# Kernel tuning notes

Measured on AMD Instinct MI355X. Metric: run time of the kernel, lower is better.

Reference implementation:

```python
import jax, jax.numpy as jnp
import numpy as np
import math

D_MODEL = 512
NUM_HEADS = 8
D_K = D_MODEL // NUM_HEADS
MAX_LEN = 500
BATCH = 32
SEQ = 480


def setup_inputs() -> dict:
    key = jax.random.key(0)
    ks = jax.random.split(key, 10)
    s = 0.02
    x = jax.random.normal(ks[0], (BATCH, SEQ, D_MODEL), dtype=jnp.float32)
    wq = jax.random.normal(ks[1], (D_MODEL, D_MODEL), dtype=jnp.float32) * s
    bq = jnp.zeros((D_MODEL,), jnp.float32)
    wk = jax.random.normal(ks[2], (D_MODEL, D_MODEL), dtype=jnp.float32) * s
    bk = jnp.zeros((D_MODEL,), jnp.float32)
    wv = jax.random.normal(ks[3], (D_MODEL, D_MODEL), dtype=jnp.float32) * s
    bv = jnp.zeros((D_MODEL,), jnp.float32)
    wo = jax.random.normal(ks[4], (D_MODEL, D_MODEL), dtype=jnp.float32) * s
    bo = jnp.zeros((D_MODEL,), jnp.float32)
    rel_bias = jax.random.normal(ks[5], (NUM_HEADS, MAX_LEN, MAX_LEN), dtype=jnp.float32) * 0.02
    return {"x": x, "wq": wq, "bq": bq, "wk": wk, "bk": bk, "wv": wv,
            "bv": bv, "wo": wo, "bo": bo, "rel_bias": rel_bias}


def reference(x, wq, bq, wk, bk, wv, bv, wo, bo, rel_bias):
    B, S, D = x.shape
    H, dk = NUM_HEADS, D_K
    scale = math.sqrt(dk)
    # QKV projections -> [B, H, S, dk]
    q = (x @ wq + bq).reshape(B, S, H, dk).transpose(0, 2, 1, 3)
    k = (x @ wk + bk).reshape(B, S, H, dk).transpose(0, 2, 1, 3)
    v = (x @ wv + bv).reshape(B, S, H, dk).transpose(0, 2, 1, 3)
    scores = jnp.einsum('bhqd,bhkd->bhqk', q, k) / scale
    scores = scores + rel_bias[None, :, :S, :S]
    causal = jnp.triu(jnp.ones((S, S), dtype=bool), k=1)  # True where j > i
    scores = jnp.where(causal[None, None], -jnp.inf, scores)
    attn = jax.nn.softmax(scores, axis=-1)
    ctx = jnp.einsum('bhqk,bhkd->bhqd', attn, v)
    ctx = ctx.transpose(0, 2, 1, 3).reshape(B, S, D)
    out = ctx @ wo + bo
    return out, attn.mean(axis=1)
```

## Files before the change

### kernel.cpp

```cpp
#include <hip/hip_runtime.h>
#include <hip/hip_bf16.h>


typedef unsigned short ushort_t;
typedef __attribute__((ext_vector_type(8))) short short8;
typedef __attribute__((ext_vector_type(4))) float floatx4;
typedef __attribute__((ext_vector_type(2))) __fp16 half2v;

#define NB 32
#define NS 480
#define ND 512
#define NH 8
#define NDK 64
#define MAXLEN 500
#define PSTR 36
#define SCL 0.18033688f

__device__ __forceinline__ ushort_t f2bf(float f) {
  union { float f; unsigned u; } v; v.f = f;
  unsigned r = v.u + 0x7FFFu + ((v.u >> 16) & 1u);
  return (ushort_t)(r >> 16);
}

#define GLOAD_LDS16(g, l)                                                      \
  __builtin_amdgcn_global_load_lds(                                            \
      (const __attribute__((address_space(1))) void*)(g),                      \
      (__attribute__((address_space(3))) void*)(l), 16, 0, 0)

__global__ void cvt_x(const float* __restrict__ x, ushort_t* __restrict__ xb) {
  int idx = blockIdx.x * 256 + threadIdx.x;
  float4 v = ((const float4*)x)[idx];
  ushort4 o;
  o.x = f2bf(v.x); o.y = f2bf(v.y); o.z = f2bf(v.z); o.w = f2bf(v.w);
  ((ushort4*)xb)[idx] = o;
}

__global__ void cvt_w(const float* __restrict__ wq, const float* __restrict__ wk,
                      const float* __restrict__ wv, const float* __restrict__ wo,
                      ushort_t* __restrict__ wqT, ushort_t* __restrict__ wkT,
                      ushort_t* __restrict__ wvT, ushort_t* __restrict__ woT) {
  __shared__ float t[32][33];
  int z = blockIdx.z;
  const float* w = (z == 0) ? wq : (z == 1) ? wk : (z == 2) ? wv : wo;
  ushort_t* wT = (z == 0) ? wqT : (z == 1) ? wkT : (z == 2) ? wvT : woT;
  int k0 = blockIdx.x * 32, n0 = blockIdx.y * 32;
  int tx = threadIdx.x & 31, ty = threadIdx.x >> 5;
#pragma unroll
  for (int yy = 0; yy < 4; ++yy)
    t[ty + yy * 8][tx] = w[(k0 + ty + yy * 8) * ND + n0 + tx];
  __syncthreads();
#pragma unroll
  for (int yy = 0; yy < 4; ++yy)
    wT[(n0 + ty + yy * 8) * ND + k0 + tx] = f2bf(t[tx][ty + yy * 8]);
}

__global__ void cvt_rbt(const float* __restrict__ rel_bias, float* __restrict__ rbt) {
  int kt = blockIdx.x, ib = blockIdx.y, h = blockIdx.z;
  int lm = threadIdx.x & 15, ii = threadIdx.x >> 4;
  int i = ib * 16 + ii;
  float f0 = rel_bias[((size_t)h * MAXLEN + i) * MAXLEN + kt * 32 + lm] * 1.44269504f;
  float f1 = rel_bias[((size_t)h * MAXLEN + i) * MAXLEN + kt * 32 + 16 + lm] * 1.44269504f;
  float2 o = {f0, f1};
  *(float2*)&rbt[(((size_t)h * 15 + kt) * NS + i) * 32 + 2 * lm] = o;
}

__global__ __launch_bounds__(256)
void qk_gemm(const ushort_t* __restrict__ xb,
             const ushort_t* __restrict__ wqT, const ushort_t* __restrict__ wkT,
             const float* __restrict__ bq, const float* __restrict__ bk,
             ushort_t* __restrict__ qb, ushort_t* __restrict__ kb) {
  __shared__ __align__(16) ushort_t sA[128 * 64];
  __shared__ __align__(16) ushort_t sB[128 * 64];
  const int tid = threadIdx.x;
  const int wid = tid >> 6, lane = tid & 63;
  const int lm = lane & 15, quad = lane >> 4;
  const int wr = wid >> 1, wc = wid & 1;
  const int row0 = blockIdx.x * 128;
  const int col0 = blockIdx.y * 128;
  const int z = blockIdx.z;
  const ushort_t* Bt = (z == 0) ? wqT : wkT;
  const float* bias = (z == 0) ? bq : bk;

  floatx4 zero4 = {0.f, 0.f, 0.f, 0.f};
  floatx4 acc[4][4];
#pragma unroll
  for (int i = 0; i < 4; ++i)
#pragma unroll
    for (int j = 0; j < 4; ++j) acc[i][j] = zero4;

  for (int k0 = 0; k0 < ND; k0 += 64) {
#pragma unroll
    for (int c = 0; c < 4; ++c) {
      int li = c * 256 + tid;
      int row = li >> 3, kc = li & 7;
      int kcs = kc ^ (row & 7);
      GLOAD_LDS16(xb + (row0 + row) * ND + k0 + kcs * 8, sA + (c * 256 + wid * 64) * 8);
      GLOAD_LDS16(Bt + (col0 + row) * ND + k0 + kcs * 8, sB + (c * 256 + wid * 64) * 8);
    }
    __syncthreads();
#pragma unroll
    for (int h2 = 0; h2 < 2; ++h2) {
      short8 a[4], b[4];
#pragma unroll
      for (int i = 0; i < 4; ++i) {
        int row = wr * 64 + i * 16 + lm;
        a[i] = *(const short8*)&sA[row * 64 + (((h2 << 2) | quad) ^ (lm & 7)) * 8];
      }
#pragma unroll
      for (int j = 0; j < 4; ++j) {
        int row = wc * 64 + j * 16 + lm;
        b[j] = *(const short8*)&sB[row * 64 + (((h2 << 2) | quad) ^ (lm & 7)) * 8];
      }
#pragma unroll
      for (int i = 0; i < 4; ++i)
#pragma unroll
        for (int j = 0; j < 4; ++j)
          acc[i][j] = __builtin_amdgcn_mfma_f32_16x16x32_bf16(a[i], b[j], acc[i][j], 0, 0, 0);
    }
    __syncthreads();
  }

  float bsv[4];
#pragma unroll
  for (int j = 0; j < 4; ++j) bsv[j] = bias[col0 + wc * 64 + j * 16 + lm];

#pragma unroll
  for (int i = 0; i < 4; ++i)
#pragma unroll
    for (int j = 0; j < 4; ++j)
#pragma unroll
      for (int r = 0; r < 4; ++r) {
        int m = row0 + wr * 64 + i * 16 + quad * 4 + r;
        int n = col0 + wc * 64 + j * 16 + lm;
        float val = acc[i][j][r] + bsv[j];
        int bb = m / NS, s = m - bb * NS;
        int h = n >> 6, d = n & 63;
        ushort_t o = f2bf(val);
        if (z == 0) qb[((bb * NH + h) * NS + s) * NDK + d] = o;
        else        kb[((bb * NH + h) * NS + s) * NDK + d] = o;
      }
}

__global__ __launch_bounds__(256)
void v_gemm(const ushort_t* __restrict__ xb, const ushort_t* __restrict__ wvT,
            const float* __restrict__ bv, ushort_t* __restrict__ vtil) {
  __shared__ __align__(16) ushort_t sA[128 * 64];
  __shared__ __align__(16) ushort_t sB[128 * 64];
  const int tid = threadIdx.x;
  const int wid = tid >> 6, lane = tid & 63;
  const int lm = lane & 15, quad = lane >> 4;
  const int wr = wid >> 1, wc = wid & 1;
  const int row0 = blockIdx.x * 128;
  const int col0 = blockIdx.y * 128;
  const int b = blockIdx.z;
  const ushort_t* xbb = xb + (size_t)b * NS * ND;

  floatx4 zero4 = {0.f, 0.f, 0.f, 0.f};
  floatx4 acc[4][4];
#pragma unroll
  for (int i = 0; i < 4; ++i)
#pragma unroll
    for (int j = 0; j < 4; ++j) acc[i][j] = zero4;

  for (int k0 = 0; k0 < ND; k0 += 64) {
#pragma unroll
    for (int c = 0; c < 4; ++c) {
      int li = c * 256 + tid;
      int row = li >> 3, kc = li & 7;
      int kcs = kc ^ (row & 7);
      GLOAD_LDS16(wvT + (row0 + row) * ND + k0 + kcs * 8, sA + (c * 256 + wid * 64) * 8);
      int srow = min(col0 + row, NS - 1);
      GLOAD_LDS16(xbb + srow * ND + k0 + kcs * 8, sB + (c * 256 + wid * 64) * 8);
    }
    __syncthreads();
#pragma unroll
    for (int h2 = 0; h2 < 2; ++h2) {
      short8 a[4], b2[4];
#pragma unroll
      for (int i = 0; i < 4; ++i) {
        int row = wr * 64 + i * 16 + lm;
        a[i] = *(const short8*)&sA[row * 64 + (((h2 << 2) | quad) ^ (lm & 7)) * 8];
      }
#pragma unroll
      for (int j = 0; j < 4; ++j) {
        int row = wc * 64 + j * 16 + lm;
        b2[j] = *(const short8*)&sB[row * 64 + (((h2 << 2) | quad) ^ (lm & 7)) * 8];
      }
#pragma unroll
      for (int i = 0; i < 4; ++i)
#pragma unroll
        for (int j = 0; j < 4; ++j)
          acc[i][j] = __builtin_amdgcn_mfma_f32_16x16x32_bf16(a[i], b2[j], acc[i][j], 0, 0, 0);
    }
    __syncthreads();
  }

#pragma unroll
  for (int i = 0; i < 4; ++i)
#pragma unroll
    for (int r = 0; r < 4; ++r) {
      int m = row0 + wr * 64 + i * 16 + quad * 4 + r;
      float bias = bv[m];
#pragma unroll
      for (int j = 0; j < 4; ++j) {
        int n = col0 + wc * 64 + j * 16 + lm;
        if (n < NS) {
          size_t idx = (((size_t)b * NH + (m >> 6)) * 15 + (n >> 5)) * 2048 +
                       (m & 63) * 32 + (n & 31);
          vtil[idx] = f2bf(acc[i][j][r] + bias);
        }
      }
    }
}

__global__ __launch_bounds__(256)
void flash_attn(const ushort_t* __restrict__ qb, const ushort_t* __restrict__ kb,
                const ushort_t* __restrict__ vtil, const float* __restrict__ rbt,
                ushort_t* __restrict__ ctxb, float* __restrict__ cst,
                uint4* __restrict__ pscr) {
  const int bh = blockIdx.x;
  const int b = bh >> 3, h = bh & 7;
  const int tid = threadIdx.x;
  const int wid = tid >> 6, lane = tid & 63;
  const int lm = lane & 15, quad = lane >> 4;

  __shared__ __align__(16) ushort_t sP[4][32 * PSTR];

  const int t = 14 - (blockIdx.y * 4 + wid);
  if (t < 0) return;
  const int nkt = t + 1;

  const ushort_t* qh = qb + (size_t)bh * NS * NDK;
  const ushort_t* kh = kb + (size_t)bh * NS * NDK;
  const ushort_t* vb = vtil + (size_t)bh * 15 * 2048;
  const float* rb = rbt + (size_t)h * 15 * NS * 32;
  uint4* pp = pscr + ((size_t)(bh * 120 + (t * (t + 1)) / 2)) * 128 + lane;

  short8 aq[2][2];
#pragma unroll
  for (int g = 0; g < 2; ++g) {
    aq[g][0] = *(const short8*)&qh[(t * 32 + g * 16 + lm) * NDK + quad * 8];
    aq[g][1] = *(const short8*)&qh[(t * 32 + g * 16 + lm) * NDK + 32 + quad * 8];
  }

  float lsum[2][4];
  floatx4 O[2][4];
  floatx4 zero4 = {0.f, 0.f, 0.f, 0.f};
#pragma unroll
  for (int g = 0; g < 2; ++g) {
#pragma unroll
    for (int r = 0; r < 4; ++r) lsum[g][r] = 0.f;
#pragma unroll
    for (int jd = 0; jd < 4; ++jd) O[g][jd] = zero4;
  }

  for (int kt = 0; kt < nkt; ++kt) {
    const int kvA = kt * 32 + lm;
    const int kvB = kvA + 16;
    short8 bkA0 = *(const short8*)&kh[kvA * NDK + quad * 8];
    short8 bkA1 = *(const short8*)&kh[kvA * NDK + 32 + quad * 8];
    short8 bkB0 = *(const short8*)&kh[kvB * NDK + quad * 8];
    short8 bkB1 = *(const short8*)&kh[kvB * NDK + 32 + quad * 8];
    short8 bv2[4];
#pragma unroll
    for (int jd = 0; jd < 4; ++jd)
      bv2[jd] = *(const short8*)&vb[kt * 2048 + (jd * 16 + lm) * 32 + quad * 8];
    float2 bb[2][4];
#pragma unroll
    for (int g = 0; g < 2; ++g)
#pragma unroll
      for (int r = 0; r < 4; ++r) {
        int i = t * 32 + g * 16 + quad * 4 + r;
        bb[g][r] = *(const float2*)&rb[((size_t)kt * NS + i) * 32 + 2 * lm];
      }

    floatx4 sA[2], sB[2];
    __builtin_amdgcn_s_setprio(1);
#pragma unroll
    for (int g = 0; g < 2; ++g) {
      floatx4 s = zero4;
      s = __builtin_amdgcn_mfma_f32_16x16x32_bf16(aq[g][0], bkA0, s, 0, 0, 0);
      s = __builtin_amdgcn_mfma_f32_16x16x32_bf16(aq[g][1], bkA1, s, 0, 0, 0);
      sA[g] = s;
      s = zero4;
      s = __builtin_amdgcn_mfma_f32_16x16x32_bf16(aq[g][0], bkB0, s, 0, 0, 0);
      s = __builtin_amdgcn_mfma_f32_16x16x32_bf16(aq[g][1], bkB1, s, 0, 0, 0);
      sB[g] = s;
    }
    __builtin_amdgcn_s_setprio(0);

    const bool diag = (kt == t);
#pragma unroll
    for (int g = 0; g < 2; ++g) {
      unsigned pw[4];
#pragma unroll
      for (int r = 0; r < 4; ++r) {
        float p0 = __builtin_amdgcn_exp2f(fmaf(sA[g][r], SCL, bb[g][r].x));
        float p1 = __builtin_amdgcn_exp2f(fmaf(sB[g][r], SCL, bb[g][r].y));
        if (diag) {
          int i = t * 32 + g * 16 + quad * 4 + r;
          if (kvA > i) p0 = 0.f;
          if (kvB > i) p1 = 0.f;
        }
        lsum[g][r] += p0 + p1;
        unsigned pk;
        asm("v_cvt_pk_bf16_f32 %0, %1, %2" : "=v"(pk) : "v"(p0), "v"(p1));
        sP[wid][(g * 16 + quad * 4 + r) * PSTR + lm] = (ushort_t)(pk & 0xffffu);
        sP[wid][(g * 16 + quad * 4 + r) * PSTR + 16 + lm] = (ushort_t)(pk >> 16);
        half2v hp = __builtin_amdgcn_cvt_pkrtz(p0, p1);
        pw[r] = *(unsigned*)&hp;
      }
      uint4 pq = {pw[0], pw[1], pw[2], pw[3]};
      pp[(size_t)kt * 128 + g * 64] = pq;
    }

    __builtin_amdgcn_s_setprio(1);
#pragma unroll
    for (int g = 0; g < 2; ++g) {
      short8 ap = *(const short8*)&sP[wid][(g * 16 + lm) * PSTR + quad * 8];
#pragma unroll
      for (int jd = 0; jd < 4; ++jd)
        O[g][jd] = __builtin_amdgcn_mfma_f32_16x16x32_bf16(ap, bv2[jd], O[g][jd], 0, 0, 0);
    }
    __builtin_amdgcn_s_setprio(0);
  }

#pragma unroll
  for (int off = 1; off < 16; off <<= 1)
#pragma unroll
    for (int g = 0; g < 2; ++g)
#pragma unroll
      for (int r = 0; r < 4; ++r) lsum[g][r] += __shfl_xor(lsum[g][r], off, 64);

#pragma unroll
  for (int g = 0; g < 2; ++g) {
    float rinv[4];
#pragma unroll
    for (int r = 0; r < 4; ++r) rinv[r] = 1.f / lsum[g][r];
#pragma unroll
    for (int jd = 0; jd < 4; ++jd)
#pragma unroll
      for (int r = 0; r < 4; ++r) {
        int i = t * 32 + g * 16 + quad * 4 + r;
        ctxb[((size_t)b * NS + i) * ND + h * NDK + jd * 16 + lm] =
            f2bf(O[g][jd][r] * rinv[r]);
      }
    if (lm == 0) {
#pragma unroll
      for (int r = 0; r < 4; ++r) {
        int i = t * 32 + g * 16 + quad * 4 + r;
        cst[(size_t)bh * NS + i] = rinv[r];
      }
    }
  }
}

__global__ __launch_bounds__(64)
void attn_mean_p(const uint4* __restrict__ pscr, const float* __restrict__ cst,
                 float* __restrict__ am) {
  const int b = blockIdx.x, t = blockIdx.y, kt = blockIdx.z;
  const int lane = threadIdx.x;
  const int lm = lane & 15, quad = lane >> 4;
  float* outp = am + ((size_t)b * NS + t * 32) * NS + (size_t)kt * 32;
  if (kt > t) {
#pragma unroll
    for (int g = 0; g < 2; ++g)
#pragma unroll
      for (int r = 0; r < 4; ++r) {
        int row = g * 16 + quad * 4 + r;
        outp[(size_t)row * NS + lm] = 0.f;
        outp[(size_t)row * NS + 16 + lm] = 0.f;
      }
    return;
  }
  const int m = (t * (t + 1)) / 2 + kt;
  float a0[2][4], a1[2][4];
#pragma unroll
  for (int g = 0; g < 2; ++g)
#pragma unroll
    for (int r = 0; r < 4; ++r) { a0[g][r] = 0.f; a1[g][r] = 0.f; }

#pragma unroll
  for (int h = 0; h < NH; ++h) {
    const uint4* pp = pscr + ((size_t)(b * NH + h) * 120 + m) * 128 + lane;
    uint4 q0 = pp[0];
    uint4 q1 = pp[64];
    unsigned pu[8] = {q0.x, q0.y, q0.z, q0.w, q1.x, q1.y, q1.z, q1.w};
    const float* cp = cst + (size_t)(b * NH + h) * NS + t * 32 + quad * 4;
    float4 rv0 = *(const float4*)cp;
    float4 rv1 = *(const float4*)(cp + 16);
    float rv[8] = {rv0.x, rv0.y, rv0.z, rv0.w, rv1.x, rv1.y, rv1.z, rv1.w};
#pragma unroll
    for (int g = 0; g < 2; ++g)
#pragma unroll
      for (int r = 0; r < 4; ++r) {
        half2v hp = *(half2v*)&pu[g * 4 + r];
        a0[g][r] = fmaf((float)hp.x, rv[g * 4 + r], a0[g][r]);
        a1[g][r] = fmaf((float)hp.y, rv[g * 4 + r], a1[g][r]);
      }
  }

#pragma unroll
  for (int g = 0; g < 2; ++g)
#pragma unroll
    for (int r = 0; r < 4; ++r) {
      int row = g * 16 + quad * 4 + r;
      outp[(size_t)row * NS + lm] = a0[g][r] * 0.125f;
      outp[(size_t)row * NS + 16 + lm] = a1[g][r] * 0.125f;
    }
}

__global__ __launch_bounds__(256)
void out_gemm(const ushort_t* __restrict__ ctxb, const ushort_t* __restrict__ woT,
              const float* __restrict__ bo, float* __restrict__ out) {
  __shared__ __align__(16) ushort_t sA[128 * 64];
  __shared__ __align__(16) ushort_t sB[128 * 64];
  const int tid = threadIdx.x;
  const int wid = tid >> 6, lane = tid & 63;
  const int lm = lane & 15, quad = lane >> 4;
  const int wr = wid >> 1, wc = wid & 1;
  const int row0 = blockIdx.x * 128;
  const int col0 = blockIdx.y * 128;

  floatx4 zero4 = {0.f, 0.f, 0.f, 0.f};
  floatx4 acc[4][4];
#pragma unroll
  for (int i = 0; i < 4; ++i)
#pragma unroll
    for (int j = 0; j < 4; ++j) acc[i][j] = zero4;

  for (int k0 = 0; k0 < ND; k0 += 64) {
#pragma unroll
    for (int c = 0; c < 4; ++c) {
      int li = c * 256 + tid;
      int row = li >> 3, kc = li & 7;
      int kcs = kc ^ (row & 7);
      GLOAD_LDS16(ctxb + (row0 + row) * ND + k0 + kcs * 8, sA + (c * 256 + wid * 64) * 8);
      GLOAD_LDS16(woT + (col0 + row) * ND + k0 + kcs * 8, sB + (c * 256 + wid * 64) * 8);
    }
    __syncthreads();
#pragma unroll
    for (int h2 = 0; h2 < 2; ++h2) {
      short8 a[4], b[4];
#pragma unroll
      for (int i = 0; i < 4; ++i) {
        int row = wr * 64 + i * 16 + lm;
        a[i] = *(const short8*)&sA[row * 64 + (((h2 << 2) | quad) ^ (lm & 7)) * 8];
      }
#pragma unroll
      for (int j = 0; j < 4; ++j) {
        int row = wc * 64 + j * 16 + lm;
        b[j] = *(const short8*)&sB[row * 64 + (((h2 << 2) | quad) ^ (lm & 7)) * 8];
      }
#pragma unroll
      for (int i = 0; i < 4; ++i)
#pragma unroll
        for (int j = 0; j < 4; ++j)
          acc[i][j] = __builtin_amdgcn_mfma_f32_16x16x32_bf16(a[i], b[j], acc[i][j], 0, 0, 0);
    }
    __syncthreads();
  }

  float bsv[4];
#pragma unroll
  for (int j = 0; j < 4; ++j) bsv[j] = bo[col0 + wc * 64 + j * 16 + lm];

#pragma unroll
  for (int i = 0; i < 4; ++i)
#pragma unroll
    for (int j = 0; j < 4; ++j)
#pragma unroll
      for (int r = 0; r < 4; ++r) {
        int m = row0 + wr * 64 + i * 16 + quad * 4 + r;
        int n = col0 + wc * 64 + j * 16 + lm;
        out[m * ND + n] = acc[i][j][r] + bsv[j];
      }
}

extern "C" void kernel_launch(void* const* d_in, const int* in_sizes, int n_in,
                              void* d_out, int out_size, void* d_ws, size_t ws_size,
                              hipStream_t stream) {
  const float* x  = (const float*)d_in[0];
  const float* wq = (const float*)d_in[1];
  const float* bq = (const float*)d_in[2];
  const float* wk = (const float*)d_in[3];
  const float* bk = (const float*)d_in[4];
  const float* wv = (const float*)d_in[5];
  const float* bv = (const float*)d_in[6];
  const float* wo = (const float*)d_in[7];
  const float* bo = (const float*)d_in[8];
  const float* rel_bias = (const float*)d_in[9];

  char* w = (char*)d_ws;
  ushort_t* xb  = (ushort_t*)w;
  ushort_t* wqT = (ushort_t*)(w + 15728640);
  ushort_t* wkT = wqT + 262144;
  ushort_t* wvT = wkT + 262144;
  ushort_t* woT = wvT + 262144;
  ushort_t* qb  = (ushort_t*)(w + 15728640 + 4 * 524288);
  ushort_t* kb  = qb + 7864320;
  ushort_t* vtil = kb + 7864320;
  ushort_t* ctxb = vtil + 7864320;
  float* cstat = (float*)(w + 80740352);
  uint4* pscr = (uint4*)(w + 81264640);
  float* rbt = (float*)w;

  float* out0 = (float*)d_out;
  float* attn_mean = out0 + 7864320;

  cvt_x<<<dim3(7680), dim3(256), 0, stream>>>(x, xb);
  cvt_w<<<dim3(16, 16, 4), dim3(256), 0, stream>>>(wq, wk, wv, wo, wqT, wkT, wvT, woT);
  qk_gemm<<<dim3(120, 4, 2), dim3(256), 0, stream>>>(xb, wqT, wkT, bq, bk, qb, kb);
  v_gemm<<<dim3(4, 4, 32), dim3(256), 0, stream>>>(xb, wvT, bv, vtil);
  cvt_rbt<<<dim3(15, 30, 8), dim3(256), 0, stream>>>(rel_bias, rbt);
  flash_attn<<<dim3(256, 4), dim3(256), 0, stream>>>(qb, kb, vtil, rbt, ctxb, cstat, pscr);
  attn_mean_p<<<dim3(32, 15, 15), dim3(64), 0, stream>>>(pscr, cstat, attn_mean);
  out_gemm<<<dim3(120, 4), dim3(256), 0, stream>>>(ctxb, woT, bo, out0);
}
```

Baseline: 230.9 us.

## Fuse conversion and QKV GEMM launches; pair causal query tiles per wave

Merges the x and weight bf16 conversion kernels into one launch, and the Q/K and V projection GEMMs into one launch dispatched on blockIdx.z. In flash attention each wave now processes two query tiles (t and 13-t, with one slot taking the last tile), so every wave does an equal amount of causal work and the grid is halved. The aim is to cut launch overhead and causal load imbalance, at the cost of fewer concurrent waves for latency hiding and some idle padding blocks in the fused GEMM.

```diff
diff --git a/kernel.cpp b/kernel.cpp
--- a/kernel.cpp
+++ b/kernel.cpp
@@ -27,23 +27,27 @@
       (const __attribute__((address_space(1))) void*)(g),                      \
       (__attribute__((address_space(3))) void*)(l), 16, 0, 0)
 
-__global__ void cvt_x(const float* __restrict__ x, ushort_t* __restrict__ xb) {
-  int idx = blockIdx.x * 256 + threadIdx.x;
-  float4 v = ((const float4*)x)[idx];
-  ushort4 o;
-  o.x = f2bf(v.x); o.y = f2bf(v.y); o.z = f2bf(v.z); o.w = f2bf(v.w);
-  ((ushort4*)xb)[idx] = o;
-}
-
-__global__ void cvt_w(const float* __restrict__ wq, const float* __restrict__ wk,
-                      const float* __restrict__ wv, const float* __restrict__ wo,
-                      ushort_t* __restrict__ wqT, ushort_t* __restrict__ wkT,
-                      ushort_t* __restrict__ wvT, ushort_t* __restrict__ woT) {
+__global__ __launch_bounds__(256)
+void cvt_xw(const float* __restrict__ x, const float* __restrict__ wq,
+            const float* __restrict__ wk, const float* __restrict__ wv,
+            const float* __restrict__ wo, ushort_t* __restrict__ xb,
+            ushort_t* __restrict__ wqT, ushort_t* __restrict__ wkT,
+            ushort_t* __restrict__ wvT, ushort_t* __restrict__ woT) {
   __shared__ float t[32][33];
-  int z = blockIdx.z;
+  const int bid = blockIdx.x;
+  if (bid < 7680) {
+    int idx = bid * 256 + threadIdx.x;
+    float4 v = ((const float4*)x)[idx];
+    ushort4 o;
+    o.x = f2bf(v.x); o.y = f2bf(v.y); o.z = f2bf(v.z); o.w = f2bf(v.w);
+    ((ushort4*)xb)[idx] = o;
+    return;
+  }
+  const int q = bid - 7680;
+  const int z = q >> 8;
   const float* w = (z == 0) ? wq : (z == 1) ? wk : (z == 2) ? wv : wo;
   ushort_t* wT = (z == 0) ? wqT : (z == 1) ? wkT : (z == 2) ? wvT : woT;
-  int k0 = blockIdx.x * 32, n0 = blockIdx.y * 32;
+  int k0 = (q & 15) * 32, n0 = ((q >> 4) & 15) * 32;
   int tx = threadIdx.x & 31, ty = threadIdx.x >> 5;
 #pragma unroll
   for (int yy = 0; yy < 4; ++yy)
@@ -65,21 +69,20 @@
 }
 
 __global__ __launch_bounds__(256)
-void qk_gemm(const ushort_t* __restrict__ xb,
-             const ushort_t* __restrict__ wqT, const ushort_t* __restrict__ wkT,
-             const float* __restrict__ bq, const float* __restrict__ bk,
-             ushort_t* __restrict__ qb, ushort_t* __restrict__ kb) {
+void qkv_gemm(const ushort_t* __restrict__ xb,
+              const ushort_t* __restrict__ wqT, const ushort_t* __restrict__ wkT,
+              const ushort_t* __restrict__ wvT,
+              const float* __restrict__ bq, const float* __restrict__ bk,
+              const float* __restrict__ bv,
+              ushort_t* __restrict__ qb, ushort_t* __restrict__ kb,
+              ushort_t* __restrict__ vtil) {
   __shared__ __align__(16) ushort_t sA[128 * 64];
   __shared__ __align__(16) ushort_t sB[128 * 64];
   const int tid = threadIdx.x;
   const int wid = tid >> 6, lane = tid & 63;
   const int lm = lane & 15, quad = lane >> 4;
   const int wr = wid >> 1, wc = wid & 1;
-  const int row0 = blockIdx.x * 128;
-  const int col0 = blockIdx.y * 128;
   const int z = blockIdx.z;
-  const ushort_t* Bt = (z == 0) ? wqT : wkT;
-  const float* bias = (z == 0) ? bq : bk;
 
   floatx4 zero4 = {0.f, 0.f, 0.f, 0.f};
   floatx4 acc[4][4];
@@ -88,129 +91,120 @@
 #pragma unroll
     for (int j = 0; j < 4; ++j) acc[i][j] = zero4;
 
-  for (int k0 = 0; k0 < ND; k0 += 64) {
-#pragma unroll
-    for (int c = 0; c < 4; ++c) {
-      int li = c * 256 + tid;
-      int row = li >> 3, kc = li & 7;
-      int kcs = kc ^ (row & 7);
-      GLOAD_LDS16(xb + (row0 + row) * ND + k0 + kcs * 8, sA + (c * 256 + wid * 64) * 8);
-      GLOAD_LDS16(Bt + (col0 + row) * ND + k0 + kcs * 8, sB + (c * 256 + wid * 64) * 8);
-    }
-    __syncthreads();
-#pragma unroll
-    for (int h2 = 0; h2 < 2; ++h2) {
-      short8 a[4], b[4];
-#pragma unroll
-      for (int i = 0; i < 4; ++i) {
-        int row = wr * 64 + i * 16 + lm;
-        a[i] = *(const short8*)&sA[row * 64 + (((h2 << 2) | quad) ^ (lm & 7)) * 8];
-      }
-#pragma unroll
-      for (int j = 0; j < 4; ++j) {
-        int row = wc * 64 + j * 16 + lm;
-        b[j] = *(const short8*)&sB[row * 64 + (((h2 << 2) | quad) ^ (lm & 7)) * 8];
-      }
-#pragma unroll
-      for (int i = 0; i < 4; ++i)
-#pragma unroll
-        for (int j = 0; j < 4; ++j)
-          acc[i][j] = __builtin_amdgcn_mfma_f32_16x16x32_bf16(a[i], b[j], acc[i][j], 0, 0, 0);
-    }
-    __syncthreads();
-  }
-
-  float bsv[4];
-#pragma unroll
-  for (int j = 0; j < 4; ++j) bsv[j] = bias[col0 + wc * 64 + j * 16 + lm];
-
-#pragma unroll
-  for (int i = 0; i < 4; ++i)
-#pragma unroll
-    for (int j = 0; j < 4; ++j)
+  if (z < 2) {
+    if (blockIdx.x >= 120) return;
+    const int row0 = blockIdx.x * 128;
+    const int col0 = blockIdx.y * 128;
+    const ushort_t* Bt = (z == 0) ? wqT : wkT;
+    const float* bias = (z == 0) ? bq : bk;
+
+    for (int k0 = 0; k0 < ND; k0 += 64) {
+#pragma unroll
+      for (int c = 0; c < 4; ++c) {
+        int li = c * 256 + tid;
+        int row = li >> 3, kc = li & 7;
+        int kcs = kc ^ (row & 7);
+        GLOAD_LDS16(xb + (row0 + row) * ND + k0 + kcs * 8, sA + (c * 256 + wid * 64) * 8);
+        GLOAD_LDS16(Bt + (col0 + row) * ND + k0 + kcs * 8, sB + (c * 256 + wid * 64) * 8);
+      }
+      __syncthreads();
+#pragma unroll
+      for (int h2 = 0; h2 < 2; ++h2) {
+        short8 a[4], b[4];
+#pragma unroll
+        for (int i = 0; i < 4; ++i) {
+          int row = wr * 64 + i * 16 + lm;
+          a[i] = *(const short8*)&sA[row * 64 + (((h2 << 2) | quad) ^ (lm & 7)) * 8];
+        }
+#pragma unroll
+        for (int j = 0; j < 4; ++j) {
+          int row = wc * 64 + j * 16 + lm;
+          b[j] = *(const short8*)&sB[row * 64 + (((h2 << 2) | quad) ^ (lm & 7)) * 8];
+        }
+#pragma unroll
+        for (int i = 0; i < 4; ++i)
+#pragma unroll
+          for (int j = 0; j < 4; ++j)
+            acc[i][j] = __builtin_amdgcn_mfma_f32_16x16x32_bf16(a[i], b[j], acc[i][j], 0, 0, 0);
+      }
+      __syncthreads();
+    }
+
+    float bsv[4];
+#pragma unroll
+    for (int j = 0; j < 4; ++j) bsv[j] = bias[col0 + wc * 64 + j * 16 + lm];
+
+#pragma unroll
+    for (int i = 0; i < 4; ++i)
+#pragma unroll
+      for (int j = 0; j < 4; ++j)
+#pragma unroll
+        for (int r = 0; r < 4; ++r) {
+          int m = row0 + wr * 64 + i * 16 + quad * 4 + r;
+          int n = col0 + wc * 64 + j * 16 + lm;
+          float val = acc[i][j][r] + bsv[j];
+          int bb = m / NS, s = m - bb * NS;
+          int h = n >> 6, d = n & 63;
+          ushort_t o = f2bf(val);
+          if (z == 0) qb[((bb * NH + h) * NS + s) * NDK + d] = o;
+          else        kb[((bb * NH + h) * NS + s) * NDK + d] = o;
+        }
+  } else {
+    const int b = blockIdx.x >> 2;
+    const int row0 = (blockIdx.x & 3) * 128;
+    const int col0 = blockIdx.y * 128;
+    const ushort_t* xbb = xb + (size_t)b * NS * ND;
+
+    for (int k0 = 0; k0 < ND; k0 += 64) {
+#pragma unroll
+      for (int c = 0; c < 4; ++c) {
+        int li = c * 256 + tid;
+        int row = li >> 3, kc = li & 7;
+        int kcs = kc ^ (row & 7);
+        GLOAD_LDS16(wvT + (row0 + row) * ND + k0 + kcs * 8, sA + (c * 256 + wid * 64) * 8);
+        int srow = min(col0 + row, NS - 1);
+        GLOAD_LDS16(xbb + srow * ND + k0 + kcs * 8, sB + (c * 256 + wid * 64) * 8);
+      }
+      __syncthreads();
+#pragma unroll
+      for (int h2 = 0; h2 < 2; ++h2) {
+        short8 a[4], b2[4];
+#pragma unroll
+        for (int i = 0; i < 4; ++i) {
+          int row = wr * 64 + i * 16 + lm;
+          a[i] = *(const short8*)&sA[row * 64 + (((h2 << 2) | quad) ^ (lm & 7)) * 8];
+        }
+#pragma unroll
+        for (int j = 0; j < 4; ++j) {
+          int row = wc * 64 + j * 16 + lm;
+          b2[j] = *(const short8*)&sB[row * 64 + (((h2 << 2) | quad) ^ (lm & 7)) * 8];
+        }
+#pragma unroll
+        for (int i = 0; i < 4; ++i)
+#pragma unroll
+          for (int j = 0; j < 4; ++j)
+            acc[i][j] = __builtin_amdgcn_mfma_f32_16x16x32_bf16(a[i], b2[j], acc[i][j], 0, 0, 0);
+      }
+      __syncthreads();
+    }
+
+#pragma unroll
+    for (int i = 0; i < 4; ++i)
 #pragma unroll
       for (int r = 0; r < 4; ++r) {
         int m = row0 + wr * 64 + i * 16 + quad * 4 + r;
-        int n = col0 + wc * 64 + j * 16 + lm;
-        float val = acc[i][j][r] + bsv[j];
-        int bb = m / NS, s = m - bb * NS;
-        int h = n >> 6, d = n & 63;
-        ushort_t o = f2bf(val);
-        if (z == 0) qb[((bb * NH + h) * NS + s) * NDK + d] = o;
-        else        kb[((bb * NH + h) * NS + s) * NDK + d] = o;
-      }
-}
-
-__global__ __launch_bounds__(256)
-void v_gemm(const ushort_t* __restrict__ xb, const ushort_t* __restrict__ wvT,
-            const float* __restrict__ bv, ushort_t* __restrict__ vtil) {
-  __shared__ __align__(16) ushort_t sA[128 * 64];
-  __shared__ __align__(16) ushort_t sB[128 * 64];
-  const int tid = threadIdx.x;
-  const int wid = tid >> 6, lane = tid & 63;
-  const int lm = lane & 15, quad = lane >> 4;
-  const int wr = wid >> 1, wc = wid & 1;
-  const int row0 = blockIdx.x * 128;
-  const int col0 = blockIdx.y * 128;
-  const int b = blockIdx.z;
-  const ushort_t* xbb = xb + (size_t)b * NS * ND;
-
-  floatx4 zero4 = {0.f, 0.f, 0.f, 0.f};
-  floatx4 acc[4][4];
-#pragma unroll
-  for (int i = 0; i < 4; ++i)
-#pragma unroll
-    for (int j = 0; j < 4; ++j) acc[i][j] = zero4;
-
-  for (int k0 = 0; k0 < ND; k0 += 64) {
-#pragma unroll
-    for (int c = 0; c < 4; ++c) {
-      int li = c * 256 + tid;
-      int row = li >> 3, kc = li & 7;
-      int kcs = kc ^ (row & 7);
-      GLOAD_LDS16(wvT + (row0 + row) * ND + k0 + kcs * 8, sA + (c * 256 + wid * 64) * 8);
-      int srow = min(col0 + row, NS - 1);
-      GLOAD_LDS16(xbb + srow * ND + k0 + kcs * 8, sB + (c * 256 + wid * 64) * 8);
-    }
-    __syncthreads();
-#pragma unroll
-    for (int h2 = 0; h2 < 2; ++h2) {
-      short8 a[4], b2[4];
-#pragma unroll
-      for (int i = 0; i < 4; ++i) {
-        int row = wr * 64 + i * 16 + lm;
-        a[i] = *(const short8*)&sA[row * 64 + (((h2 << 2) | quad) ^ (lm & 7)) * 8];
-      }
-#pragma unroll
-      for (int j = 0; j < 4; ++j) {
-        int row = wc * 64 + j * 16 + lm;
-        b2[j] = *(const short8*)&sB[row * 64 + (((h2 << 2) | quad) ^ (lm & 7)) * 8];
-      }
-#pragma unroll
-      for (int i = 0; i < 4; ++i)
-#pragma unroll
-        for (int j = 0; j < 4; ++j)
-          acc[i][j] = __builtin_amdgcn_mfma_f32_16x16x32_bf16(a[i], b2[j], acc[i][j], 0, 0, 0);
-    }
-    __syncthreads();
+        float bias = bv[m];
+#pragma unroll
+        for (int j = 0; j < 4; ++j) {
+          int n = col0 + wc * 64 + j * 16 + lm;
+          if (n < NS) {
+            size_t idx = (((size_t)b * NH + (m >> 6)) * 15 + (n >> 5)) * 2048 +
+                         (m & 63) * 32 + (n & 31);
+            vtil[idx] = f2bf(acc[i][j][r] + bias);
+          }
+        }
+      }
   }
-
-#pragma unroll
-  for (int i = 0; i < 4; ++i)
-#pragma unroll
-    for (int r = 0; r < 4; ++r) {
-      int m = row0 + wr * 64 + i * 16 + quad * 4 + r;
-      float bias = bv[m];
-#pragma unroll
-      for (int j = 0; j < 4; ++j) {
-        int n = col0 + wc * 64 + j * 16 + lm;
-        if (n < NS) {
-          size_t idx = (((size_t)b * NH + (m >> 6)) * 15 + (n >> 5)) * 2048 +
-                       (m & 63) * 32 + (n & 31);
-          vtil[idx] = f2bf(acc[i][j][r] + bias);
-        }
-      }
-    }
 }
 
 __global__ __launch_bounds__(256)
@@ -226,130 +220,137 @@
 
   __shared__ __align__(16) ushort_t sP[4][32 * PSTR];
 
-  const int t = 14 - (blockIdx.y * 4 + wid);
-  if (t < 0) return;
-  const int nkt = t + 1;
+  const int slot = blockIdx.y * 4 + wid;
+  const int tA = (slot == 7) ? 14 : slot;
+  const int tB = (slot == 7) ? -1 : 13 - slot;
 
   const ushort_t* qh = qb + (size_t)bh * NS * NDK;
   const ushort_t* kh = kb + (size_t)bh * NS * NDK;
   const ushort_t* vb = vtil + (size_t)bh * 15 * 2048;
   const float* rb = rbt + (size_t)h * 15 * NS * 32;
-  uint4* pp = pscr + ((size_t)(bh * 120 + (t * (t + 1)) / 2)) * 128 + lane;
-
-  short8 aq[2][2];
-#pragma unroll
-  for (int g = 0; g < 2; ++g) {
-    aq[g][0] = *(const short8*)&qh[(t * 32 + g * 16 + lm) * NDK + quad * 8];
-    aq[g][1] = *(const short8*)&qh[(t * 32 + g * 16 + lm) * NDK + 32 + quad * 8];
-  }
-
-  float lsum[2][4];
-  floatx4 O[2][4];
-  floatx4 zero4 = {0.f, 0.f, 0.f, 0.f};
-#pragma unroll
-  for (int g = 0; g < 2; ++g) {
-#pragma unroll
-    for (int r = 0; r < 4; ++r) lsum[g][r] = 0.f;
-#pragma unroll
-    for (int jd = 0; jd < 4; ++jd) O[g][jd] = zero4;
-  }
-
-  for (int kt = 0; kt < nkt; ++kt) {
-    const int kvA = kt * 32 + lm;
-    const int kvB = kvA + 16;
-    short8 bkA0 = *(const short8*)&kh[kvA * NDK + quad * 8];
-    short8 bkA1 = *(const short8*)&kh[kvA * NDK + 32 + quad * 8];
-    short8 bkB0 = *(const short8*)&kh[kvB * NDK + quad * 8];
-    short8 bkB1 = *(const short8*)&kh[kvB * NDK + 32 + quad * 8];
-    short8 bv2[4];
-#pragma unroll
-    for (int jd = 0; jd < 4; ++jd)
-      bv2[jd] = *(const short8*)&vb[kt * 2048 + (jd * 16 + lm) * 32 + quad * 8];
-    float2 bb[2][4];
-#pragma unroll
-    for (int g = 0; g < 2; ++g)
-#pragma unroll
-      for (int r = 0; r < 4; ++r) {
-        int i = t * 32 + g * 16 + quad * 4 + r;
-        bb[g][r] = *(const float2*)&rb[((size_t)kt * NS + i) * 32 + 2 * lm];
-      }
-
-    floatx4 sA[2], sB[2];
-    __builtin_amdgcn_s_setprio(1);
+
+#pragma unroll 1
+  for (int ti = 0; ti < 2; ++ti) {
+    const int t = (ti == 0) ? tA : tB;
+    if (t < 0) break;
+    const int nkt = t + 1;
+    uint4* pp = pscr + ((size_t)(bh * 120 + (t * (t + 1)) / 2)) * 128 + lane;
+
+    short8 aq[2][2];
 #pragma unroll
     for (int g = 0; g < 2; ++g) {
-      floatx4 s = zero4;
-      s = __builtin_amdgcn_mfma_f32_16x16x32_bf16(aq[g][0], bkA0, s, 0, 0, 0);
-      s = __builtin_amdgcn_mfma_f32_16x16x32_bf16(aq[g][1], bkA1, s, 0, 0, 0);
-      sA[g] = s;
-      s = zero4;
-      s = __builtin_amdgcn_mfma_f32_16x16x32_bf16(aq[g][0], bkB0, s, 0, 0, 0);
-      s = __builtin_amdgcn_mfma_f32_16x16x32_bf16(aq[g][1], bkB1, s, 0, 0, 0);
-      sB[g] = s;
-    }
-    __builtin_amdgcn_s_setprio(0);
-
-    const bool diag = (kt == t);
+      aq[g][0] = *(const short8*)&qh[(t * 32 + g * 16 + lm) * NDK + quad * 8];
+      aq[g][1] = *(const short8*)&qh[(t * 32 + g * 16 + lm) * NDK + 32 + quad * 8];
+    }
+
+    float lsum[2][4];
+    floatx4 O[2][4];
+    floatx4 zero4 = {0.f, 0.f, 0.f, 0.f};
 #pragma unroll
     for (int g = 0; g < 2; ++g) {
-      unsigned pw[4];
-#pragma unroll
-      for (int r = 0; r < 4; ++r) {
-        float p0 = __builtin_amdgcn_exp2f(fmaf(sA[g][r], SCL, bb[g][r].x));
-        float p1 = __builtin_amdgcn_exp2f(fmaf(sB[g][r], SCL, bb[g][r].y));
-        if (diag) {
+#pragma unroll
+      for (int r = 0; r < 4; ++r) lsum[g][r] = 0.f;
+#pragma unroll
+      for (int jd = 0; jd < 4; ++jd) O[g][jd] = zero4;
+    }
+
+    for (int kt = 0; kt < nkt; ++kt) {
+      const int kvA = kt * 32 + lm;
+      const int kvB = kvA + 16;
+      short8 bkA0 = *(const short8*)&kh[kvA * NDK + quad * 8];
+      short8 bkA1 = *(const short8*)&kh[kvA * NDK + 32 + quad * 8];
+      short8 bkB0 = *(const short8*)&kh[kvB * NDK + quad * 8];
+      short8 bkB1 = *(const short8*)&kh[kvB * NDK + 32 + quad * 8];
+      short8 bv2[4];
+#pragma unroll
+      for (int jd = 0; jd < 4; ++jd)
+        bv2[jd] = *(const short8*)&vb[kt * 2048 + (jd * 16 + lm) * 32 + quad * 8];
+      float2 bb[2][4];
+#pragma unroll
+      for (int g = 0; g < 2; ++g)
+#pragma unroll
+        for (int r = 0; r < 4; ++r) {
           int i = t * 32 + g * 16 + quad * 4 + r;
-          if (kvA > i) p0 = 0.f;
-          if (kvB > i) p1 = 0.f;
-        }
-        lsum[g][r] += p0 + p1;
-        unsigned pk;
-        asm("v_cvt_pk_bf16_f32 %0, %1, %2" : "=v"(pk) : "v"(p0), "v"(p1));
-        sP[wid][(g * 16 + quad * 4 + r) * PSTR + lm] = (ushort_t)(pk & 0xffffu);
-        sP[wid][(g * 16 + quad * 4 + r) * PSTR + 16 + lm] = (ushort_t)(pk >> 16);
-        half2v hp = __builtin_amdgcn_cvt_pkrtz(p0, p1);
-        pw[r] = *(unsigned*)&hp;
-      }
-      uint4 pq = {pw[0], pw[1], pw[2], pw[3]};
-      pp[(size_t)kt * 128 + g * 64] = pq;
-    }
-
-    __builtin_amdgcn_s_setprio(1);
+          bb[g][r] = *(const float2*)&rb[((size_t)kt * NS + i) * 32 + 2 * lm];
+        }
+
+      floatx4 sA[2], sB[2];
+      __builtin_amdgcn_s_setprio(1);
+#pragma unroll
+      for (int g = 0; g < 2; ++g) {
+        floatx4 s = zero4;
+        s = __builtin_amdgcn_mfma_f32_16x16x32_bf16(aq[g][0], bkA0, s, 0, 0, 0);
+        s = __builtin_amdgcn_mfma_f32_16x16x32_bf16(aq[g][1], bkA1, s, 0, 0, 0);
+        sA[g] = s;
+        s = zero4;
+        s = __builtin_amdgcn_mfma_f32_16x16x32_bf16(aq[g][0], bkB0, s, 0, 0, 0);
+        s = __builtin_amdgcn_mfma_f32_16x16x32_bf16(aq[g][1], bkB1, s, 0, 0, 0);
+        sB[g] = s;
+      }
+      __builtin_amdgcn_s_setprio(0);
+
+      const bool diag = (kt == t);
+#pragma unroll
+      for (int g = 0; g < 2; ++g) {
+        unsigned pw[4];
+#pragma unroll
+        for (int r = 0; r < 4; ++r) {
+          float p0 = __builtin_amdgcn_exp2f(fmaf(sA[g][r], SCL, bb[g][r].x));
+          float p1 = __builtin_amdgcn_exp2f(fmaf(sB[g][r], SCL, bb[g][r].y));
+          if (diag) {
+            int i = t * 32 + g * 16 + quad * 4 + r;
+            if (kvA > i) p0 = 0.f;
+            if (kvB > i) p1 = 0.f;
+          }
+          lsum[g][r] += p0 + p1;
+          unsigned pk;
+          asm("v_cvt_pk_bf16_f32 %0, %1, %2" : "=v"(pk) : "v"(p0), "v"(p1));
+          sP[wid][(g * 16 + quad * 4 + r) * PSTR + lm] = (ushort_t)(pk & 0xffffu);
+          sP[wid][(g * 16 + quad * 4 + r) * PSTR + 16 + lm] = (ushort_t)(pk >> 16);
+          half2v hp = __builtin_amdgcn_cvt_pkrtz(p0, p1);
+          pw[r] = *(unsigned*)&hp;
+        }
+        uint4 pq = {pw[0], pw[1], pw[2], pw[3]};
+        pp[(size_t)kt * 128 + g * 64] = pq;
+      }
+
+      __builtin_amdgcn_s_setprio(1);
+#pragma unroll
+      for (int g = 0; g < 2; ++g) {
+        short8 ap = *(const short8*)&sP[wid][(g * 16 + lm) * PSTR + quad * 8];
+#pragma unroll
+        for (int jd = 0; jd < 4; ++jd)
+          O[g][jd] = __builtin_amdgcn_mfma_f32_16x16x32_bf16(ap, bv2[jd], O[g][jd], 0, 0, 0);
+      }
+      __builtin_amdgcn_s_setprio(0);
+    }
+
+#pragma unroll
+    for (int off = 1; off < 16; off <<= 1)
+#pragma unroll
+      for (int g = 0; g < 2; ++g)
+#pragma unroll
+        for (int r = 0; r < 4; ++r) lsum[g][r] += __shfl_xor(lsum[g][r], off, 64);
+
 #pragma unroll
     for (int g = 0; g < 2; ++g) {
-      short8 ap = *(const short8*)&sP[wid][(g * 16 + lm) * PSTR + quad * 8];
+      float rinv[4];
+#pragma unroll
+      for (int r = 0; r < 4; ++r) rinv[r] = 1.f / lsum[g][r];
 #pragma unroll
       for (int jd = 0; jd < 4; ++jd)
-        O[g][jd] = __builtin_amdgcn_mfma_f32_16x16x32_bf16(ap, bv2[jd], O[g][jd], 0, 0, 0);
-    }
-    __builtin_amdgcn_s_setprio(0);
-  }
-
-#pragma unroll
-  for (int off = 1; off < 16; off <<= 1)
-#pragma unroll
-    for (int g = 0; g < 2; ++g)
-#pragma unroll
-      for (int r = 0; r < 4; ++r) lsum[g][r] += __shfl_xor(lsum[g][r], off, 64);
-
-#pragma unroll
-  for (int g = 0; g < 2; ++g) {
-    float rinv[4];
-#pragma unroll
-    for (int r = 0; r < 4; ++r) rinv[r] = 1.f / lsum[g][r];
-#pragma unroll
-    for (int jd = 0; jd < 4; ++jd)
-#pragma unroll
-      for (int r = 0; r < 4; ++r) {
-        int i = t * 32 + g * 16 + quad * 4 + r;
-        ctxb[((size_t)b * NS + i) * ND + h * NDK + jd * 16 + lm] =
-            f2bf(O[g][jd][r] * rinv[r]);
-      }
-    if (lm == 0) {
-#pragma unroll
-      for (int r = 0; r < 4; ++r) {
-        int i = t * 32 + g * 16 + quad * 4 + r;
-        cst[(size_t)bh * NS + i] = rinv[r];
+#pragma unroll
+        for (int r = 0; r < 4; ++r) {
+          int i = t * 32 + g * 16 + quad * 4 + r;
+          ctxb[((size_t)b * NS + i) * ND + h * NDK + jd * 16 + lm] =
+              f2bf(O[g][jd][r] * rinv[r]);
+        }
+      if (lm == 0) {
+#pragma unroll
+        for (int r = 0; r < 4; ++r) {
+          int i = t * 32 + g * 16 + quad * 4 + r;
+          cst[(size_t)bh * NS + i] = rinv[r];
+        }
       }
     }
   }
@@ -508,12 +509,11 @@
   float* out0 = (float*)d_out;
   float* attn_mean = out0 + 7864320;
 
-  cvt_x<<<dim3(7680), dim3(256), 0, stream>>>(x, xb);
-  cvt_w<<<dim3(16, 16, 4), dim3(256), 0, stream>>>(wq, wk, wv, wo, wqT, wkT, wvT, woT);
-  qk_gemm<<<dim3(120, 4, 2), dim3(256), 0, stream>>>(xb, wqT, wkT, bq, bk, qb, kb);
-  v_gemm<<<dim3(4, 4, 32), dim3(256), 0, stream>>>(xb, wvT, bv, vtil);
+  cvt_xw<<<dim3(8704), dim3(256), 0, stream>>>(x, wq, wk, wv, wo, xb, wqT, wkT, wvT, woT);
+  qkv_gemm<<<dim3(128, 4, 3), dim3(256), 0, stream>>>(xb, wqT, wkT, wvT, bq, bk, bv,
+                                                      qb, kb, vtil);
   cvt_rbt<<<dim3(15, 30, 8), dim3(256), 0, stream>>>(rel_bias, rbt);
-  flash_attn<<<dim3(256, 4), dim3(256), 0, stream>>>(qb, kb, vtil, rbt, ctxb, cstat, pscr);
+  flash_attn<<<dim3(256, 2), dim3(256), 0, stream>>>(qb, kb, vtil, rbt, ctxb, cstat, pscr);
   attn_mean_p<<<dim3(32, 15, 15), dim3(64), 0, stream>>>(pscr, cstat, attn_mean);
   out_gemm<<<dim3(120, 4), dim3(256), 0, stream>>>(ctxb, woT, bo, out0);
 }
```

Result: no change. 226.4 us (-2.0%).
